# Optimization experiments

Hardware: AMD Instinct MI355X
Metric: run time of the kernel (lower is better)

## Reference

```python
import jax, jax.numpy as jnp
import numpy as np

N_NODES = 100000
N_EDGES = 1600000
IN_CH = 128
OUT_CH = 64

def setup_inputs() -> dict:
    key = jax.random.key(0)
    k = jax.random.split(key, 7)
    x = jax.random.normal(k[0], (N_NODES, IN_CH), dtype=jnp.float32)
    edge_index = jax.random.randint(k[1], (2, N_EDGES), 0, N_NODES, dtype=jnp.int64)
    neg_edge_index = jax.random.randint(k[2], (2, N_EDGES), 0, N_NODES, dtype=jnp.int64)
    # GCNConv weight [in, out] + bias, Linear classifier [2*out, 2] + bias
    W = jax.random.normal(k[3], (IN_CH, OUT_CH), dtype=jnp.float32) / np.sqrt(IN_CH)
    b = jnp.zeros((OUT_CH,), dtype=jnp.float32)
    Wc = jax.random.normal(k[4], (2 * OUT_CH, 2), dtype=jnp.float32) / np.sqrt(2 * OUT_CH)
    bc = jnp.zeros((2,), dtype=jnp.float32)
    return {"x": x, "edge_index": edge_index, "neg_edge_index": neg_edge_index,
            "W": W, "b": b, "Wc": Wc, "bc": bc}

def reference(x, edge_index, neg_edge_index, W, b, Wc, bc):
    N = x.shape[0]
    # --- GCNConv: linear transform, add self-loops, symmetric deg normalization ---
    h = x @ W                                   # [N, out]
    loops = jnp.arange(N, dtype=edge_index.dtype)
    row = jnp.concatenate([edge_index[0], loops])   # source
    col = jnp.concatenate([edge_index[1], loops])   # target
    deg = jax.ops.segment_sum(jnp.ones(col.shape, h.dtype), col, num_segments=N)
    dinv = jnp.where(deg > 0, jax.lax.rsqrt(deg), 0.0)
    norm = dinv[row] * dinv[col]                # [E+N]
    agg = jax.ops.segment_sum(h[row] * norm[:, None], col, num_segments=N)
    z = jax.nn.relu(agg + b)                    # [N, out]
    # --- edge feature gather (pos + neg edges) + linear classifier ---
    total = jnp.concatenate([edge_index, neg_edge_index], axis=1)  # [2, 2E]
    feats = jnp.concatenate([z[total[0]], z[total[1]]], axis=1)    # [2E, 2*out]
    return feats @ Wc + bc                      # [2E, 2]
```

## Files before the change

### kernel.cpp

```cpp
#include <hip/hip_runtime.h>

#define IN_CH 128
#define OUT_CH 64
#define MAXBKT 256
#define CAPB   9216
#define CAPB_PAD 18432
#define CHUNK  3328

typedef __attribute__((ext_vector_type(8))) short short8v;
typedef __attribute__((ext_vector_type(4))) float float4v;

union Pack { short8v s8; unsigned u[4]; };

__device__ __forceinline__ unsigned short f2bf(float f) {
    unsigned u = __float_as_uint(f);
    return (unsigned short)((u + 0x7fffu + ((u >> 16) & 1u)) >> 16);
}
__device__ __forceinline__ unsigned pk2(float a, float b) {
    return ((unsigned)f2bf(b) << 16) | (unsigned)f2bf(a);
}
__device__ __forceinline__ float bflo(unsigned d) { return __uint_as_float(d << 16); }
__device__ __forceinline__ float bfhi(unsigned d) { return __uint_as_float(d & 0xffff0000u); }

__global__ void k_zero_cnt(unsigned* __restrict__ cnt, int n) {
    int i = blockIdx.x * blockDim.x + threadIdx.x;
    if (i < n) cnt[i] = 0u;
}

__global__ __launch_bounds__(256) void k_binA(const int* __restrict__ ei,
                                              unsigned* __restrict__ bucketCount,
                                              unsigned* __restrict__ binned,
                                              int E, int nbkt) {
    __shared__ unsigned hist[MAXBKT];
    __shared__ unsigned resv[MAXBKT];
    __shared__ int colS[CHUNK];
    int tid = threadIdx.x;
    int start = blockIdx.x * CHUNK;
    int end = start + CHUNK; if (end > E) end = E;
    int cnt = end - start;

    for (int i = tid; i < MAXBKT; i += 256) hist[i] = 0u;
    __syncthreads();

    for (int i = tid; i < cnt; i += 256) {
        int c = ei[E + start + i];
        colS[i] = c;
        atomicAdd(&hist[c >> 9], 1u);
    }
    __syncthreads();

    if (tid < nbkt) {
        resv[tid] = atomicAdd(&bucketCount[tid], hist[tid]);
        hist[tid] = 0u;
    }
    __syncthreads();

    for (int i = tid; i < cnt; i += 256) {
        int c = colS[i];
        int r = ei[start + i];
        int bkt = c >> 9;
        unsigned rank = atomicAdd(&hist[bkt], 1u);
        unsigned idx = resv[bkt] + rank;
        if (idx < CAPB)
            binned[(size_t)bkt * CAPB + idx] = ((unsigned)r << 9) | (unsigned)(c & 511);
    }
}

__global__ __launch_bounds__(1024) void k_csrB(const unsigned* __restrict__ binned,
                                               const unsigned* __restrict__ bucketCount,
                                               int* __restrict__ rows,
                                               unsigned* __restrict__ offs,
                                               unsigned* __restrict__ degPad,
                                               float* __restrict__ dinv, int N, int nbkt) {
    __shared__ unsigned hist[512];
    __shared__ unsigned dpad[512];
    __shared__ unsigned excl[512];
    __shared__ unsigned stage[CAPB];
    int tid = threadIdx.x;
    int b = blockIdx.x;
    unsigned cnt = bucketCount[b];
    if (cnt > (unsigned)CAPB) cnt = (unsigned)CAPB;
    size_t gbase = (size_t)b * CAPB_PAD;
    int nodeBase = b << 9;
    int nn = N - nodeBase; if (nn > 512) nn = 512;

    for (int i = tid; i < 512; i += 1024) hist[i] = 0u;
    __syncthreads();

    const unsigned* src = binned + (size_t)b * CAPB;
    for (unsigned i = tid; i < cnt; i += 1024) {
        unsigned p = src[i];
        stage[i] = p;
        atomicAdd(&hist[p & 511u], 1u);
    }
    __syncthreads();

    if (tid < 512) {
        unsigned d = hist[tid];
        unsigned dp = (d + 15u) & ~15u;
        dpad[tid] = dp;
        excl[tid] = dp;
    }
    __syncthreads();
    for (int d = 1; d < 512; d <<= 1) {
        unsigned x = 0u;
        if (tid < 512) x = excl[tid] + ((tid >= d) ? excl[tid - d] : 0u);
        __syncthreads();
        if (tid < 512) excl[tid] = x;
        __syncthreads();
    }
    if (tid < 512) excl[tid] -= dpad[tid];
    __syncthreads();

    if (tid < nn) {
        unsigned d = hist[tid];
        offs[nodeBase + tid]   = (unsigned)gbase + excl[tid];
        degPad[nodeBase + tid] = dpad[tid];
        dinv[nodeBase + tid]   = rsqrtf((float)d + 1.0f);
    }
    __syncthreads();
    for (int i = tid; i < 512; i += 1024) hist[i] = 0u;
    __syncthreads();

    for (unsigned i = tid; i < cnt; i += 1024) {
        unsigned p = stage[i];
        unsigned c = p & 511u;
        unsigned r = atomicAdd(&hist[c], 1u);
        rows[gbase + excl[c] + r] = (int)(p >> 9);
    }
    __syncthreads();
    if (tid < nn) {
        unsigned d = hist[tid], dp = dpad[tid];
        size_t base = gbase + excl[tid];
        for (unsigned p = d; p < dp; ++p) rows[base + p] = N;
    }
}

__global__ __launch_bounds__(256) void k_gemm_h(const float* __restrict__ x,
                                                const float* __restrict__ W,
                                                const float* __restrict__ dinv,
                                                unsigned short* __restrict__ hs,
                                                int N, int nChunks) {
    __shared__ float Wl[IN_CH * 66];
    int tid = threadIdx.x;
    int wid = tid >> 6;
    int l   = tid & 63;
    int g   = l >> 4;
    int m   = l & 15;

    if (blockIdx.x == 0 && tid < 32)
        ((unsigned*)hs)[((size_t)N << 5) + tid] = 0u;

    const float4* W4 = (const float4*)W;
#pragma unroll
    for (int j = 0; j < 8; ++j) {
        int i4 = tid + j * 256;
        float4 w = W4[i4];
        int i = i4 * 4;
        int k = i >> 6, c = i & 63;
        float* dst = Wl + k * 66 + c;
        dst[0] = w.x; dst[1] = w.y; dst[2] = w.z; dst[3] = w.w;
    }
    __syncthreads();

    short8v bf[4][4];
#pragma unroll
    for (int s = 0; s < 4; ++s)
#pragma unroll
        for (int t = 0; t < 4; ++t) {
            Pack p;
#pragma unroll
            for (int jj = 0; jj < 4; ++jj) {
                int k = s * 32 + g * 8 + 2 * jj;
                float f0 = Wl[(k + 0) * 66 + t * 16 + m];
                float f1 = Wl[(k + 1) * 66 + t * 16 + m];
                p.u[jj] = pk2(f0, f1);
            }
            bf[s][t] = p.s8;
        }

    const float4* x4 = (const float4*)x;
    for (int chunk = blockIdx.x; chunk < nChunks; chunk += gridDim.x) {
        int R0 = chunk * 64 + wid * 16;
        int rowA = R0 + m; if (rowA > N - 1) rowA = N - 1;
        float4v acc[4];
#pragma unroll
        for (int t = 0; t < 4; ++t) acc[t] = (float4v){0.f, 0.f, 0.f, 0.f};

#pragma unroll
        for (int s = 0; s < 4; ++s) {
            const float4* ap = x4 + (size_t)rowA * 32 + s * 8 + g * 2;
            float4 a0 = ap[0];
            float4 a1 = ap[1];
            Pack pa;
            pa.u[0] = pk2(a0.x, a0.y);
            pa.u[1] = pk2(a0.z, a0.w);
            pa.u[2] = pk2(a1.x, a1.y);
            pa.u[3] = pk2(a1.z, a1.w);
#pragma unroll
            for (int t = 0; t < 4; ++t)
                acc[t] = __builtin_amdgcn_mfma_f32_16x16x32_bf16(pa.s8, bf[s][t], acc[t], 0, 0, 0);
        }

        int rbase = R0 + g * 4;
        float4 dv = *(const float4*)(dinv + rbase);
#pragma unroll
        for (int r = 0; r < 4; ++r) {
            int row = rbase + r;
            if (row < N) {
                float dvr = (r == 0) ? dv.x : (r == 1) ? dv.y : (r == 2) ? dv.z : dv.w;
#pragma unroll
                for (int t = 0; t < 4; ++t)
                    hs[(size_t)row * OUT_CH + t * 16 + m] = f2bf(acc[t][r] * dvr);
            }
        }
    }
}

__global__ __launch_bounds__(256) void k_gather(const unsigned* __restrict__ offs,
                                                const unsigned* __restrict__ degPad,
                                                const int* __restrict__ rows,
                                                const unsigned* __restrict__ hsd,
                                                const float* __restrict__ dinv,
                                                const float* __restrict__ b,
                                                const float* __restrict__ Wc,
                                                float* __restrict__ u,
                                                float* __restrict__ v, int n) {
    int lane = threadIdx.x & 63;
    int half = lane >> 5;
    int l32  = lane & 31;
    int node = blockIdx.x * (blockDim.x >> 6) + (threadIdx.x >> 6);
    if (node >= n) return;
    unsigned start = offs[node];
    unsigned cntP = degPad[node];
    const int* rp = rows + start;

    unsigned ds = hsd[((size_t)node << 5) + l32];
    float acc0 = half ? 0.f : bflo(ds);
    float acc1 = half ? 0.f : bfhi(ds);

    for (unsigned j0 = 0; j0 < cntP; j0 += 64) {
        unsigned rem = cntP - j0;
        unsigned np = rem < 64u ? rem : 64u;
        int myidx = rp[j0 + (lane < (int)np ? lane : 0)];

        for (unsigned t0 = 0; t0 < np; t0 += 16) {
            int rr[8];
#pragma unroll
            for (int s = 0; s < 8; ++s)
                rr[s] = __shfl(myidx, (int)t0 + 2 * s + half);
            unsigned dd[8];
#pragma unroll
            for (int s = 0; s < 8; ++s)
                dd[s] = hsd[((size_t)rr[s] << 5) + l32];
#pragma unroll
            for (int s = 0; s < 8; ++s) {
                acc0 += bflo(dd[s]);
                acc1 += bfhi(dd[s]);
            }
        }
    }

    acc0 += __shfl_xor(acc0, 32);
    acc1 += __shfl_xor(acc1, 32);

    float di = dinv[node];
    float2 bv = ((const float2*)b)[l32];
    float z0 = fmaxf(fmaf(acc0, di, bv.x), 0.f);
    float z1 = fmaxf(fmaf(acc1, di, bv.y), 0.f);

    float4 w = ((const float4*)(Wc + (half ? 128 : 0)))[l32];
    float p0 = z0 * w.x + z1 * w.z;
    float p1 = z0 * w.y + z1 * w.w;
#pragma unroll
    for (int off = 16; off > 0; off >>= 1) {
        p0 += __shfl_xor(p0, off);
        p1 += __shfl_xor(p1, off);
    }
    float2 r; r.x = p0; r.y = p1;
    if (lane == 0)  ((float2*)u)[node] = r;
    if (lane == 32) ((float2*)v)[node] = r;
}

__global__ void k_edges(const int* __restrict__ ei, const int* __restrict__ nei,
                        const float* __restrict__ u, const float* __restrict__ v,
                        const float* __restrict__ bc, float* __restrict__ out, int E) {
    int i = blockIdx.x * blockDim.x + threadIdx.x;
    int quads = E >> 1;
    if (i >= quads) return;
    int halfQ = quads >> 1;
    const int* base = (i < halfQ) ? ei : nei;
    int pi = (i < halfQ) ? i : i - halfQ;
    int4 ss = ((const int4*)base)[pi];
    int4 dd = ((const int4*)(base + E))[pi];
    float2 u0 = ((const float2*)u)[ss.x];
    float2 u1 = ((const float2*)u)[ss.y];
    float2 u2 = ((const float2*)u)[ss.z];
    float2 u3 = ((const float2*)u)[ss.w];
    float2 v0 = ((const float2*)v)[dd.x];
    float2 v1 = ((const float2*)v)[dd.y];
    float2 v2 = ((const float2*)v)[dd.z];
    float2 v3 = ((const float2*)v)[dd.w];
    float b0 = bc[0], b1 = bc[1];
    float4 r0, r1;
    r0.x = u0.x + v0.x + b0;  r0.y = u0.y + v0.y + b1;
    r0.z = u1.x + v1.x + b0;  r0.w = u1.y + v1.y + b1;
    r1.x = u2.x + v2.x + b0;  r1.y = u2.y + v2.y + b1;
    r1.z = u3.x + v3.x + b0;  r1.w = u3.y + v3.y + b1;
    ((float4*)out)[2 * i + 0] = r0;
    ((float4*)out)[2 * i + 1] = r1;
}

extern "C" void kernel_launch(void* const* d_in, const int* in_sizes, int n_in,
                              void* d_out, int out_size, void* d_ws, size_t ws_size,
                              hipStream_t stream) {
    const float* x   = (const float*)d_in[0];
    const int*   ei  = (const int*)d_in[1];
    const int*   nei = (const int*)d_in[2];
    const float* W   = (const float*)d_in[3];
    const float* b   = (const float*)d_in[4];
    const float* Wc  = (const float*)d_in[5];
    const float* bc  = (const float*)d_in[6];
    float* out = (float*)d_out;

    const int N = in_sizes[0] / IN_CH;
    const int E = in_sizes[1] / 2;
    const int nbkt = (N + 511) >> 9;
    const int nChunks = (N + 63) / 64;

    char* ws = (char*)d_ws;
    size_t off = 0;
    unsigned short* hs = (unsigned short*)(ws + off); off += ((size_t)N + 1) * OUT_CH * 2;
    unsigned* binned = (unsigned*)(ws + off); off += (size_t)MAXBKT * CAPB * 4;
    int*      rows   = (int*)(ws + off);      off += (size_t)MAXBKT * CAPB_PAD * 4;
    unsigned* offs   = (unsigned*)(ws + off); off += (size_t)N * 4;
    unsigned* degP   = (unsigned*)(ws + off); off += (size_t)N * 4;
    float*    dinv   = (float*)(ws + off);    off += (size_t)N * 4;
    float*    u      = (float*)(ws + off);    off += (size_t)N * 2 * 4;
    float*    v      = (float*)(ws + off);    off += (size_t)N * 2 * 4;
    unsigned* bucketCount = (unsigned*)(ws + off); off += (size_t)MAXBKT * 4;

    k_zero_cnt<<<1, 256, 0, stream>>>(bucketCount, MAXBKT);
    k_binA<<<(E + CHUNK - 1) / CHUNK, 256, 0, stream>>>(ei, bucketCount, binned, E, nbkt);
    k_csrB<<<nbkt, 1024, 0, stream>>>(binned, bucketCount, rows, offs, degP, dinv, N, nbkt);
    k_gemm_h<<<512, 256, 0, stream>>>(x, W, dinv, hs, N, nChunks);
    k_gather<<<(N + 3) / 4, 256, 0, stream>>>(offs, degP, rows, (const unsigned*)hs, dinv, b, Wc, u, v, N);
    k_edges<<<(E / 2 + 255) / 256, 256, 0, stream>>>(ei, nei, u, v, bc, out, E);
}
```

Before: 138.3 us.

## Vectorize neighbor gather with 16-byte loads and speed up CSR scan

The gather kernel now has each wave process eight neighbors at once, with 8 lanes each loading a 16-byte chunk of a bf16 row instead of 4-byte loads. This cuts load instructions and shuffles, and the classifier projection is reworked to match. Padding per node drops from 16 to 8 rows, which reduces the dummy loads from the padding and the rows buffer size. The CSR scan is replaced by a wave-shuffle scan, and the second histogram pass reuses the counts by decrementing them, which removes several barriers. The wider gather layout needs eight accumulators and a three-step cross-group reduction per node.

```diff
diff --git a/kernel.cpp b/kernel.cpp
--- a/kernel.cpp
+++ b/kernel.cpp
@@ -4,7 +4,7 @@
 #define OUT_CH 64
 #define MAXBKT 256
 #define CAPB   9216
-#define CAPB_PAD 18432
+#define CAPB_PAD 12800
 #define CHUNK  3328
 
 typedef __attribute__((ext_vector_type(8))) short short8v;
@@ -21,6 +21,13 @@
 }
 __device__ __forceinline__ float bflo(unsigned d) { return __uint_as_float(d << 16); }
 __device__ __forceinline__ float bfhi(unsigned d) { return __uint_as_float(d & 0xffff0000u); }
+
+__device__ __forceinline__ void acc8(float* a, uint4 d) {
+    a[0] += bflo(d.x); a[1] += bfhi(d.x);
+    a[2] += bflo(d.y); a[3] += bfhi(d.y);
+    a[4] += bflo(d.z); a[5] += bfhi(d.z);
+    a[6] += bflo(d.w); a[7] += bfhi(d.w);
+}
 
 __global__ void k_zero_cnt(unsigned* __restrict__ cnt, int n) {
     int i = blockIdx.x * blockDim.x + threadIdx.x;
@@ -73,8 +80,9 @@
                                                unsigned* __restrict__ degPad,
                                                float* __restrict__ dinv, int N, int nbkt) {
     __shared__ unsigned hist[512];
-    __shared__ unsigned dpad[512];
     __shared__ unsigned excl[512];
+    __shared__ unsigned wsum[8];
+    __shared__ unsigned wexc[8];
     __shared__ unsigned stage[CAPB];
     int tid = threadIdx.x;
     int b = blockIdx.x;
@@ -95,42 +103,46 @@
     }
     __syncthreads();
 
+    unsigned d = 0, dp = 0, winc = 0;
     if (tid < 512) {
-        unsigned d = hist[tid];
-        unsigned dp = (d + 15u) & ~15u;
-        dpad[tid] = dp;
-        excl[tid] = dp;
-    }
-    __syncthreads();
-    for (int d = 1; d < 512; d <<= 1) {
-        unsigned x = 0u;
-        if (tid < 512) x = excl[tid] + ((tid >= d) ? excl[tid - d] : 0u);
-        __syncthreads();
-        if (tid < 512) excl[tid] = x;
-        __syncthreads();
-    }
-    if (tid < 512) excl[tid] -= dpad[tid];
+        d = hist[tid];
+        dp = (d + 7u) & ~7u;
+        winc = dp;
+#pragma unroll
+        for (int o = 1; o < 64; o <<= 1) {
+            unsigned t = __shfl_up(winc, o);
+            if ((tid & 63) >= o) winc += t;
+        }
+        if ((tid & 63) == 63) wsum[tid >> 6] = winc;
+    }
+    __syncthreads();
+    if (tid < 8) {
+        unsigned s = wsum[tid];
+        unsigned inc = s;
+#pragma unroll
+        for (int o = 1; o < 8; o <<= 1) {
+            unsigned t = __shfl_up(inc, o);
+            if (tid >= o) inc += t;
+        }
+        wexc[tid] = inc - s;
+    }
+    __syncthreads();
+    if (tid < 512) excl[tid] = wexc[tid >> 6] + winc - dp;
     __syncthreads();
 
     if (tid < nn) {
-        unsigned d = hist[tid];
         offs[nodeBase + tid]   = (unsigned)gbase + excl[tid];
-        degPad[nodeBase + tid] = dpad[tid];
+        degPad[nodeBase + tid] = dp;
         dinv[nodeBase + tid]   = rsqrtf((float)d + 1.0f);
     }
-    __syncthreads();
-    for (int i = tid; i < 512; i += 1024) hist[i] = 0u;
-    __syncthreads();
 
     for (unsigned i = tid; i < cnt; i += 1024) {
         unsigned p = stage[i];
         unsigned c = p & 511u;
-        unsigned r = atomicAdd(&hist[c], 1u);
-        rows[gbase + excl[c] + r] = (int)(p >> 9);
-    }
-    __syncthreads();
+        unsigned r = atomicAdd(&hist[c], 0xFFFFFFFFu);
+        rows[gbase + excl[c] + r - 1u] = (int)(p >> 9);
+    }
     if (tid < nn) {
-        unsigned d = hist[tid], dp = dpad[tid];
         size_t base = gbase + excl[tid];
         for (unsigned p = d; p < dp; ++p) rows[base + p] = N;
     }
@@ -217,69 +229,95 @@
     }
 }
 
-__global__ __launch_bounds__(256) void k_gather(const unsigned* __restrict__ offs,
+__global__ __launch_bounds__(512) void k_gather(const unsigned* __restrict__ offs,
                                                 const unsigned* __restrict__ degPad,
                                                 const int* __restrict__ rows,
-                                                const unsigned* __restrict__ hsd,
+                                                const uint4* __restrict__ hsq,
                                                 const float* __restrict__ dinv,
-                                                const float* __restrict__ b,
+                                                const float* __restrict__ bv,
                                                 const float* __restrict__ Wc,
                                                 float* __restrict__ u,
                                                 float* __restrict__ v, int n) {
     int lane = threadIdx.x & 63;
-    int half = lane >> 5;
-    int l32  = lane & 31;
+    int e8 = lane >> 3;
+    int l8 = lane & 7;
     int node = blockIdx.x * (blockDim.x >> 6) + (threadIdx.x >> 6);
     if (node >= n) return;
     unsigned start = offs[node];
     unsigned cntP = degPad[node];
     const int* rp = rows + start;
 
-    unsigned ds = hsd[((size_t)node << 5) + l32];
-    float acc0 = half ? 0.f : bflo(ds);
-    float acc1 = half ? 0.f : bfhi(ds);
+    float acc[8];
+    {
+        uint4 d = hsq[(size_t)node * 8 + l8];
+        bool s = (e8 == 0);
+        acc[0] = s ? bflo(d.x) : 0.f;  acc[1] = s ? bfhi(d.x) : 0.f;
+        acc[2] = s ? bflo(d.y) : 0.f;  acc[3] = s ? bfhi(d.y) : 0.f;
+        acc[4] = s ? bflo(d.z) : 0.f;  acc[5] = s ? bfhi(d.z) : 0.f;
+        acc[6] = s ? bflo(d.w) : 0.f;  acc[7] = s ? bfhi(d.w) : 0.f;
+    }
 
     for (unsigned j0 = 0; j0 < cntP; j0 += 64) {
         unsigned rem = cntP - j0;
         unsigned np = rem < 64u ? rem : 64u;
-        int myidx = rp[j0 + (lane < (int)np ? lane : 0)];
-
-        for (unsigned t0 = 0; t0 < np; t0 += 16) {
-            int rr[8];
-#pragma unroll
-            for (int s = 0; s < 8; ++s)
-                rr[s] = __shfl(myidx, (int)t0 + 2 * s + half);
-            unsigned dd[8];
-#pragma unroll
-            for (int s = 0; s < 8; ++s)
-                dd[s] = hsd[((size_t)rr[s] << 5) + l32];
-#pragma unroll
-            for (int s = 0; s < 8; ++s) {
-                acc0 += bflo(dd[s]);
-                acc1 += bfhi(dd[s]);
-            }
-        }
-    }
-
-    acc0 += __shfl_xor(acc0, 32);
-    acc1 += __shfl_xor(acc1, 32);
+        int myidx = rp[j0 + ((unsigned)lane < np ? (unsigned)lane : 0u)];
+
+        unsigned t0 = 0;
+        for (; t0 + 16 <= np; t0 += 16) {
+            int ra = __shfl(myidx, (int)t0 + e8);
+            int rb = __shfl(myidx, (int)(t0 + 8) + e8);
+            uint4 da = hsq[(size_t)ra * 8 + l8];
+            uint4 db = hsq[(size_t)rb * 8 + l8];
+            acc8(acc, da);
+            acc8(acc, db);
+        }
+        if (t0 < np) {
+            int ra = __shfl(myidx, (int)t0 + e8);
+            uint4 da = hsq[(size_t)ra * 8 + l8];
+            acc8(acc, da);
+        }
+    }
+
+#pragma unroll
+    for (int j = 0; j < 8; ++j) {
+        acc[j] += __shfl_xor(acc[j], 8);
+        acc[j] += __shfl_xor(acc[j], 16);
+        acc[j] += __shfl_xor(acc[j], 32);
+    }
 
     float di = dinv[node];
-    float2 bv = ((const float2*)b)[l32];
-    float z0 = fmaxf(fmaf(acc0, di, bv.x), 0.f);
-    float z1 = fmaxf(fmaf(acc1, di, bv.y), 0.f);
-
-    float4 w = ((const float4*)(Wc + (half ? 128 : 0)))[l32];
-    float p0 = z0 * w.x + z1 * w.z;
-    float p1 = z0 * w.y + z1 * w.w;
-#pragma unroll
-    for (int off = 16; off > 0; off >>= 1) {
-        p0 += __shfl_xor(p0, off);
-        p1 += __shfl_xor(p1, off);
-    }
-    float2 r; r.x = p0; r.y = p1;
-    if (lane == 0)  ((float2*)u)[node] = r;
-    if (lane == 32) ((float2*)v)[node] = r;
+    float4 b0 = ((const float4*)bv)[l8 * 2 + 0];
+    float4 b1 = ((const float4*)bv)[l8 * 2 + 1];
+    float z[8];
+    z[0] = fmaxf(fmaf(acc[0], di, b0.x), 0.f);
+    z[1] = fmaxf(fmaf(acc[1], di, b0.y), 0.f);
+    z[2] = fmaxf(fmaf(acc[2], di, b0.z), 0.f);
+    z[3] = fmaxf(fmaf(acc[3], di, b0.w), 0.f);
+    z[4] = fmaxf(fmaf(acc[4], di, b1.x), 0.f);
+    z[5] = fmaxf(fmaf(acc[5], di, b1.y), 0.f);
+    z[6] = fmaxf(fmaf(acc[6], di, b1.z), 0.f);
+    z[7] = fmaxf(fmaf(acc[7], di, b1.w), 0.f);
+
+    const float4* wcu = (const float4*)Wc + l8 * 4;
+    const float4* wcv = (const float4*)(Wc + 128) + l8 * 4;
+    float u0 = 0.f, u1 = 0.f, v0 = 0.f, v1 = 0.f;
+#pragma unroll
+    for (int q = 0; q < 4; ++q) {
+        float4 wu = wcu[q], wv = wcv[q];
+        u0 = fmaf(z[2*q], wu.x, fmaf(z[2*q+1], wu.z, u0));
+        u1 = fmaf(z[2*q], wu.y, fmaf(z[2*q+1], wu.w, u1));
+        v0 = fmaf(z[2*q], wv.x, fmaf(z[2*q+1], wv.z, v0));
+        v1 = fmaf(z[2*q], wv.y, fmaf(z[2*q+1], wv.w, v1));
+    }
+#pragma unroll
+    for (int off = 1; off <= 4; off <<= 1) {
+        u0 += __shfl_xor(u0, off);  u1 += __shfl_xor(u1, off);
+        v0 += __shfl_xor(v0, off);  v1 += __shfl_xor(v1, off);
+    }
+    if (lane == 0) {
+        float2 ru; ru.x = u0; ru.y = u1; ((float2*)u)[node] = ru;
+        float2 rv; rv.x = v0; rv.y = v1; ((float2*)v)[node] = rv;
+    }
 }
 
 __global__ void k_edges(const int* __restrict__ ei, const int* __restrict__ nei,
@@ -344,6 +382,6 @@
     k_binA<<<(E + CHUNK - 1) / CHUNK, 256, 0, stream>>>(ei, bucketCount, binned, E, nbkt);
     k_csrB<<<nbkt, 1024, 0, stream>>>(binned, bucketCount, rows, offs, degP, dinv, N, nbkt);
     k_gemm_h<<<512, 256, 0, stream>>>(x, W, dinv, hs, N, nChunks);
-    k_gather<<<(N + 3) / 4, 256, 0, stream>>>(offs, degP, rows, (const unsigned*)hs, dinv, b, Wc, u, v, N);
+    k_gather<<<(N + 7) / 8, 512, 0, stream>>>(offs, degP, rows, (const uint4*)hs, dinv, b, Wc, u, v, N);
     k_edges<<<(E / 2 + 255) / 256, 256, 0, stream>>>(ei, nei, u, v, bc, out, E);
 }
```

After: 167.0 us. +20.7%, slower.
